# Kernel tuning notes

Measured on AMD Instinct MI355X. Metric: run time of the kernel, lower is better.

## Reference

```python
import jax, jax.numpy as jnp
import numpy as np

N, E, D, H = 100000, 640000, 128, 256


def _mlp(x, w1, b1, w2, b2, w3, b3):
    x = jax.nn.relu(x @ w1.T + b1)
    x = jax.nn.relu(x @ w2.T + b2)
    return x @ w3.T + b3


def _gru(x, h, wih, whh, bih, bhh):
    gi = x @ wih.T + bih
    gh = h @ whh.T + bhh
    ir, iz, inn = jnp.split(gi, 3, axis=-1)
    hr, hz, hn = jnp.split(gh, 3, axis=-1)
    r = jax.nn.sigmoid(ir + hr)
    z = jax.nn.sigmoid(iz + hz)
    n = jnp.tanh(inn + r * hn)
    return (1.0 - z) * n + z * h


def setup_inputs() -> dict:
    key = jax.random.key(0)
    ks = jax.random.split(key, 24)
    s = lambda *shape: 0.05
    inp = {
        "node_states": jax.random.normal(ks[0], (N, D), jnp.float32),
        "edge_features": jax.random.normal(ks[1], (E, D), jnp.float32),
        "from_idx": jax.random.randint(ks[2], (E,), 0, N, jnp.int64 if jax.config.jax_enable_x64 else jnp.int32),
        "to_idx": jax.random.randint(ks[3], (E,), 0, N, jnp.int64 if jax.config.jax_enable_x64 else jnp.int32),
        "graph_idx": jax.random.randint(ks[4], (N,), 0, 16, jnp.int32),
        # message_net MLP params
        "w1": jax.random.normal(ks[5], (H, 3 * D), jnp.float32) * 0.05,
        "b1": jnp.zeros((H,), jnp.float32),
        "w2": jax.random.normal(ks[6], (H, H), jnp.float32) * 0.05,
        "b2": jnp.zeros((H,), jnp.float32),
        "w3": jax.random.normal(ks[7], (D, H), jnp.float32) * 0.05,
        "b3": jnp.zeros((D,), jnp.float32),
    }
    # three GRU cells
    for i in range(3):
        inp[f"g{i}_wih"] = jax.random.normal(ks[8 + 4 * i], (3 * D, D), jnp.float32) * 0.05
        inp[f"g{i}_whh"] = jax.random.normal(ks[9 + 4 * i], (3 * D, D), jnp.float32) * 0.05
        inp[f"g{i}_bih"] = jnp.zeros((3 * D,), jnp.float32)
        inp[f"g{i}_bhh"] = jnp.zeros((3 * D,), jnp.float32)
    return inp


def _prop_once(node_states, f_idx, t_idx, edge_features, w1, b1, w2, b2, w3, b3):
    from_states = node_states[f_idx]  # [E, D]
    to_states = node_states[t_idx]    # [E, D]
    edge_inputs = jnp.concatenate([from_states, to_states, edge_features], axis=1)  # [E, 3D]
    edge_states = _mlp(edge_inputs, w1, b1, w2, b2, w3, b3)  # [E, D]
    return jax.ops.segment_sum(edge_states, t_idx, num_segments=node_states.shape[0])


def reference(node_states, edge_features, from_idx, to_idx, graph_idx,
              w1, b1, w2, b2, w3, b3,
              g0_wih, g0_whh, g0_bih, g0_bhh,
              g1_wih, g1_whh, g1_bih, g1_bhh,
              g2_wih, g2_whh, g2_bih, g2_bhh):
    # both directions use self.message_net in the original forward
    agg = _prop_once(node_states, from_idx, to_idx, edge_features, w1, b1, w2, b2, w3, b3)
    agg = agg + _prop_once(node_states, to_idx, from_idx, edge_features, w1, b1, w2, b2, w3, b3)
    s1 = _gru(node_states, agg, g0_wih, g0_whh, g0_bih, g0_bhh)
    s2 = _gru(agg, s1, g1_wih, g1_whh, g1_bih, g1_bhh)
    s3 = _gru(s1, s2, g2_wih, g2_whh, g2_bih, g2_bhh)
    return s3
```

## Files before the change

### kernel.cpp

```cpp
#include <hip/hip_runtime.h>

#define NN 100000
#define NE 640000
#define D 128
#define HH 256
#define TD 384

typedef __bf16 bf16x8 __attribute__((ext_vector_type(8)));
typedef float f32x4 __attribute__((ext_vector_type(4)));

__device__ __forceinline__ unsigned short f2bf(float f) {
    unsigned u = __builtin_bit_cast(unsigned, f);
    u += 0x7FFFu + ((u >> 16) & 1u);
    return (unsigned short)(u >> 16);
}

__global__ void cvt_bf16_kernel(const float* __restrict__ src,
                                unsigned short* __restrict__ dst, int n) {
    int i = blockIdx.x * 256 + threadIdx.x;
    if (i < n) dst[i] = f2bf(src[i]);
}

__global__ __launch_bounds__(256, 2) void edge_mlp_kernel(
    const float* __restrict__ ns, const float* __restrict__ ef,
    const int* __restrict__ fidx, const int* __restrict__ tidx,
    const unsigned short* __restrict__ w1b, const float* __restrict__ b1,
    const unsigned short* __restrict__ w2b, const float* __restrict__ b2,
    const unsigned short* __restrict__ w3b, const float* __restrict__ b3,
    float* __restrict__ agg)
{
    __shared__ __align__(16) unsigned short chunks[96 * 128];
    __shared__ __align__(16) unsigned short hbuf[64 * 256];
    __shared__ int sF[32], sT[32];

    const int tid = threadIdx.x;
    const int e0 = blockIdx.x * 32;
    if (tid < 32) { sF[tid] = fidx[e0 + tid]; sT[tid] = tidx[e0 + tid]; }
    __syncthreads();

    {
        const int kk0 = (tid & 7) * 16;
        for (int c = tid >> 3; c < 96; c += 32) {
            const int edge = c & 31;
            const int part = c >> 5;
            const float* src = (part == 0) ? ns + (size_t)sF[edge] * D
                             : (part == 1) ? ns + (size_t)sT[edge] * D
                                           : ef + (size_t)(e0 + edge) * D;
            unsigned short* cb = chunks + c * 128;
            #pragma unroll
            for (int g = 0; g < 2; g++) {
                float4 a = *(const float4*)(src + kk0 + g * 8);
                float4 b = *(const float4*)(src + kk0 + g * 8 + 4);
                uint4 pk;
                pk.x = f2bf(a.x) | ((unsigned)f2bf(a.y) << 16);
                pk.y = f2bf(a.z) | ((unsigned)f2bf(a.w) << 16);
                pk.z = f2bf(b.x) | ((unsigned)f2bf(b.y) << 16);
                pk.w = f2bf(b.z) | ((unsigned)f2bf(b.w) << 16);
                int sw = (kk0 + g * 8) ^ ((edge & 7) << 3);
                *(uint4*)(cb + sw) = pk;
            }
        }
    }
    __syncthreads();

    const int w  = tid >> 6;
    const int l  = tid & 63;
    const int lr = l & 15;
    const int lk = l >> 4;

    f32x4 acc1[4][4];
    #pragma unroll
    for (int mt = 0; mt < 4; mt++)
        #pragma unroll
        for (int ct = 0; ct < 4; ct++) acc1[mt][ct] = (f32x4){0.f, 0.f, 0.f, 0.f};

    for (int kc = 0; kc < 12; kc++) {
        const int gk = kc * 32;
        const int c128 = gk >> 7;
        const int kk = (gk & 127) + lk * 8;
        bf16x8 af[4];
        #pragma unroll
        for (int mt = 0; mt < 4; mt++) {
            int edge = ((mt & 1) << 4) + lr;
            int dir = mt >> 1;
            int part = dir ? (c128 == 0 ? 1 : (c128 == 1 ? 0 : 2)) : c128;
            int idx = (part * 32 + edge) * 128 + (kk ^ ((edge & 7) << 3));
            af[mt] = *(const bf16x8*)(chunks + idx);
        }
        #pragma unroll
        for (int ct = 0; ct < 4; ct++) {
            int col = (w * 4 + ct) * 16 + lr;
            bf16x8 bfr = *(const bf16x8*)(w1b + col * TD + gk + lk * 8);
            #pragma unroll
            for (int mt = 0; mt < 4; mt++)
                acc1[mt][ct] = __builtin_amdgcn_mfma_f32_16x16x32_bf16(af[mt], bfr, acc1[mt][ct], 0, 0, 0);
        }
    }
    #pragma unroll
    for (int ct = 0; ct < 4; ct++) {
        int col = (w * 4 + ct) * 16 + lr;
        float bias = b1[col];
        #pragma unroll
        for (int mt = 0; mt < 4; mt++)
            #pragma unroll
            for (int j = 0; j < 4; j++) {
                int row = mt * 16 + lk * 4 + j;
                float v = acc1[mt][ct][j] + bias;
                v = v > 0.f ? v : 0.f;
                hbuf[row * 256 + (col ^ ((row & 7) << 3))] = f2bf(v);
            }
    }
    __syncthreads();

    f32x4 acc2[4][4];
    #pragma unroll
    for (int mt = 0; mt < 4; mt++)
        #pragma unroll
        for (int ct = 0; ct < 4; ct++) acc2[mt][ct] = (f32x4){0.f, 0.f, 0.f, 0.f};

    for (int kc = 0; kc < 8; kc++) {
        const int k = kc * 32 + lk * 8;
        bf16x8 af[4];
        #pragma unroll
        for (int mt = 0; mt < 4; mt++) {
            int row = mt * 16 + lr;
            af[mt] = *(const bf16x8*)(hbuf + row * 256 + (k ^ ((row & 7) << 3)));
        }
        #pragma unroll
        for (int ct = 0; ct < 4; ct++) {
            int col = (w * 4 + ct) * 16 + lr;
            bf16x8 bfr = *(const bf16x8*)(w2b + col * 256 + k);
            #pragma unroll
            for (int mt = 0; mt < 4; mt++)
                acc2[mt][ct] = __builtin_amdgcn_mfma_f32_16x16x32_bf16(af[mt], bfr, acc2[mt][ct], 0, 0, 0);
        }
    }
    __syncthreads();
    #pragma unroll
    for (int ct = 0; ct < 4; ct++) {
        int col = (w * 4 + ct) * 16 + lr;
        float bias = b2[col];
        #pragma unroll
        for (int mt = 0; mt < 4; mt++)
            #pragma unroll
            for (int j = 0; j < 4; j++) {
                int row = mt * 16 + lk * 4 + j;
                float v = acc2[mt][ct][j] + bias;
                v = v > 0.f ? v : 0.f;
                hbuf[row * 256 + (col ^ ((row & 7) << 3))] = f2bf(v);
            }
    }
    __syncthreads();

    f32x4 acc3[4][2];
    #pragma unroll
    for (int mt = 0; mt < 4; mt++) { acc3[mt][0] = (f32x4){0.f,0.f,0.f,0.f}; acc3[mt][1] = (f32x4){0.f,0.f,0.f,0.f}; }

    for (int kc = 0; kc < 8; kc++) {
        const int k = kc * 32 + lk * 8;
        bf16x8 af[4];
        #pragma unroll
        for (int mt = 0; mt < 4; mt++) {
            int row = mt * 16 + lr;
            af[mt] = *(const bf16x8*)(hbuf + row * 256 + (k ^ ((row & 7) << 3)));
        }
        #pragma unroll
        for (int ct = 0; ct < 2; ct++) {
            int col = (w * 2 + ct) * 16 + lr;
            bf16x8 bfr = *(const bf16x8*)(w3b + col * 256 + k);
            #pragma unroll
            for (int mt = 0; mt < 4; mt++)
                acc3[mt][ct] = __builtin_amdgcn_mfma_f32_16x16x32_bf16(af[mt], bfr, acc3[mt][ct], 0, 0, 0);
        }
    }

    #pragma unroll
    for (int ct = 0; ct < 2; ct++) {
        int d = (w * 2 + ct) * 16 + lr;
        float bias = b3[d];
        #pragma unroll
        for (int mt = 0; mt < 4; mt++)
            #pragma unroll
            for (int j = 0; j < 4; j++) {
                int edge = ((mt & 1) << 4) + lk * 4 + j;
                int node = (mt >> 1) ? sF[edge] : sT[edge];
                atomicAdd(agg + (size_t)node * D + d, acc3[mt][ct][j] + bias);
            }
    }
}

__global__ __launch_bounds__(256, 2) void gru_kernel(
    const float* __restrict__ x, const float* __restrict__ h,
    const unsigned short* __restrict__ wihb, const unsigned short* __restrict__ whhb,
    const float* __restrict__ bih, const float* __restrict__ bhh,
    float* __restrict__ out)
{
    __shared__ __align__(16) unsigned short xb[32 * 128];
    __shared__ __align__(16) unsigned short hb[32 * 128];
    const int tid = threadIdx.x;
    const size_t r0 = (size_t)blockIdx.x * 32;

    {
        const int row = tid >> 3;
        const int kk0 = (tid & 7) * 16;
        const float* sx = x + (r0 + row) * D + kk0;
        const float* sh = h + (r0 + row) * D + kk0;
        #pragma unroll
        for (int g = 0; g < 2; g++) {
            float4 a = *(const float4*)(sx + g * 8);
            float4 b = *(const float4*)(sx + g * 8 + 4);
            uint4 pk;
            pk.x = f2bf(a.x) | ((unsigned)f2bf(a.y) << 16);
            pk.y = f2bf(a.z) | ((unsigned)f2bf(a.w) << 16);
            pk.z = f2bf(b.x) | ((unsigned)f2bf(b.y) << 16);
            pk.w = f2bf(b.z) | ((unsigned)f2bf(b.w) << 16);
            int sw = (kk0 + g * 8) ^ ((row & 7) << 3);
            *(uint4*)(xb + row * 128 + sw) = pk;
            a = *(const float4*)(sh + g * 8);
            b = *(const float4*)(sh + g * 8 + 4);
            pk.x = f2bf(a.x) | ((unsigned)f2bf(a.y) << 16);
            pk.y = f2bf(a.z) | ((unsigned)f2bf(a.w) << 16);
            pk.z = f2bf(b.x) | ((unsigned)f2bf(b.y) << 16);
            pk.w = f2bf(b.z) | ((unsigned)f2bf(b.w) << 16);
            *(uint4*)(hb + row * 128 + sw) = pk;
        }
    }
    __syncthreads();

    const int w = tid >> 6, l = tid & 63, lr = l & 15, lk = l >> 4;

    f32x4 agi[2][3][2], agh[2][3][2];
    #pragma unroll
    for (int mt = 0; mt < 2; mt++)
        #pragma unroll
        for (int g = 0; g < 3; g++)
            #pragma unroll
            for (int t = 0; t < 2; t++) {
                agi[mt][g][t] = (f32x4){0.f,0.f,0.f,0.f};
                agh[mt][g][t] = (f32x4){0.f,0.f,0.f,0.f};
            }

    for (int kc = 0; kc < 4; kc++) {
        const int k = kc * 32 + lk * 8;
        bf16x8 ax[2], ah[2];
        #pragma unroll
        for (int mt = 0; mt < 2; mt++) {
            int row = mt * 16 + lr;
            int idx = row * 128 + (k ^ ((row & 7) << 3));
            ax[mt] = *(const bf16x8*)(xb + idx);
            ah[mt] = *(const bf16x8*)(hb + idx);
        }
        #pragma unroll
        for (int g = 0; g < 3; g++)
            #pragma unroll
            for (int t = 0; t < 2; t++) {
                int col = g * 128 + (w * 2 + t) * 16 + lr;
                bf16x8 bi = *(const bf16x8*)(wihb + col * 128 + k);
                bf16x8 bh = *(const bf16x8*)(whhb + col * 128 + k);
                #pragma unroll
                for (int mt = 0; mt < 2; mt++) {
                    agi[mt][g][t] = __builtin_amdgcn_mfma_f32_16x16x32_bf16(ax[mt], bi, agi[mt][g][t], 0, 0, 0);
                    agh[mt][g][t] = __builtin_amdgcn_mfma_f32_16x16x32_bf16(ah[mt], bh, agh[mt][g][t], 0, 0, 0);
                }
            }
    }

    #pragma unroll
    for (int t = 0; t < 2; t++) {
        const int d = (w * 2 + t) * 16 + lr;
        const float bir = bih[d], biz = bih[D + d], bin_ = bih[2 * D + d];
        const float bhr = bhh[d], bhz = bhh[D + d], bhn = bhh[2 * D + d];
        #pragma unroll
        for (int mt = 0; mt < 2; mt++)
            #pragma unroll
            for (int j = 0; j < 4; j++) {
                size_t row = r0 + mt * 16 + lk * 4 + j;
                float hv = h[row * D + d];
                float rr = agi[mt][0][t][j] + bir + agh[mt][0][t][j] + bhr;
                float zz = agi[mt][1][t][j] + biz + agh[mt][1][t][j] + bhz;
                float ni = agi[mt][2][t][j] + bin_;
                float nh = agh[mt][2][t][j] + bhn;
                float r_ = 1.f / (1.f + __expf(-rr));
                float z_ = 1.f / (1.f + __expf(-zz));
                float n_ = tanhf(ni + r_ * nh);
                out[row * D + d] = (1.f - z_) * n_ + z_ * hv;
            }
    }
}

extern "C" void kernel_launch(void* const* d_in, const int* in_sizes, int n_in,
                              void* d_out, int out_size, void* d_ws, size_t ws_size,
                              hipStream_t stream)
{
    const float* ns = (const float*)d_in[0];
    const float* ef = (const float*)d_in[1];
    const int*   fidx = (const int*)d_in[2];
    const int*   tidx = (const int*)d_in[3];
    const float* w1 = (const float*)d_in[5];
    const float* b1 = (const float*)d_in[6];
    const float* w2 = (const float*)d_in[7];
    const float* b2 = (const float*)d_in[8];
    const float* w3 = (const float*)d_in[9];
    const float* b3 = (const float*)d_in[10];
    const float* gwih_f[3] = {(const float*)d_in[11], (const float*)d_in[15], (const float*)d_in[19]};
    const float* gwhh_f[3] = {(const float*)d_in[12], (const float*)d_in[16], (const float*)d_in[20]};
    const float* gbih[3]   = {(const float*)d_in[13], (const float*)d_in[17], (const float*)d_in[21]};
    const float* gbhh[3]   = {(const float*)d_in[14], (const float*)d_in[18], (const float*)d_in[22]};

    char* ws = (char*)d_ws;
    float* agg = (float*)ws;
    float* s1  = (float*)(ws + (size_t)NN * D * 4);
    unsigned short* w1b = (unsigned short*)(ws + (size_t)2 * NN * D * 4);
    unsigned short* w2b = w1b + 256 * 384;
    unsigned short* w3b = w2b + 256 * 256;
    unsigned short* gwih[3];
    unsigned short* gwhh[3];
    {
        unsigned short* p = w3b + 128 * 256;
        for (int i = 0; i < 3; i++) { gwih[i] = p; p += 384 * 128; gwhh[i] = p; p += 384 * 128; }
    }

    auto cvt = [&](const float* s, unsigned short* dst, int n) {
        cvt_bf16_kernel<<<(n + 255) / 256, 256, 0, stream>>>(s, dst, n);
    };
    cvt(w1, w1b, 256 * 384);
    cvt(w2, w2b, 256 * 256);
    cvt(w3, w3b, 128 * 256);
    for (int i = 0; i < 3; i++) { cvt(gwih_f[i], gwih[i], 384 * 128); cvt(gwhh_f[i], gwhh[i], 384 * 128); }

    hipMemsetAsync(agg, 0, (size_t)NN * D * 4, stream);

    edge_mlp_kernel<<<NE / 32, 256, 0, stream>>>(ns, ef, fidx, tidx, w1b, b1, w2b, b2, w3b, b3, agg);

    float* s2 = (float*)d_out;
    gru_kernel<<<NN / 32, 256, 0, stream>>>(ns,  agg, gwih[0], gwhh[0], gbih[0], gbhh[0], s1);
    gru_kernel<<<NN / 32, 256, 0, stream>>>(agg, s1,  gwih[1], gwhh[1], gbih[1], gbhh[1], s2);
    gru_kernel<<<NN / 32, 256, 0, stream>>>(s1,  s2,  gwih[2], gwhh[2], gbih[2], gbhh[2], (float*)d_out);
}
```

Baseline: 1.690 ms.

## Pre-convert node/edge features to bf16 and gather via direct global-to-LDS loads

Converts node states and edge features to bf16 once up front, then gathers them into shared memory with global_load_lds 16-byte transfers instead of loading fp32 and converting per block. It also merges the chunk and hidden shared buffers into one array (adding a barrier) and raises the launch-bounds occupancy hint from 2 to 4. The aim is to halve gather bandwidth and raise occupancy, at the cost of an extra conversion pass over about 190 MB of fp32 input and a dependence on workspace size.

```diff
diff --git a/kernel.cpp b/kernel.cpp
--- a/kernel.cpp
+++ b/kernel.cpp
@@ -15,22 +15,36 @@
     return (unsigned short)(u >> 16);
 }
 
-__global__ void cvt_bf16_kernel(const float* __restrict__ src,
-                                unsigned short* __restrict__ dst, int n) {
+__device__ __forceinline__ void gl_lds16(const unsigned short* g, unsigned short* l) {
+    __builtin_amdgcn_global_load_lds((const __attribute__((address_space(1))) unsigned int*)g,
+                                     (__attribute__((address_space(3))) unsigned int*)l, 16, 0, 0);
+}
+
+__global__ void cvt8_kernel(const float* __restrict__ src,
+                            unsigned short* __restrict__ dst, int n8) {
     int i = blockIdx.x * 256 + threadIdx.x;
-    if (i < n) dst[i] = f2bf(src[i]);
-}
-
-__global__ __launch_bounds__(256, 2) void edge_mlp_kernel(
+    if (i >= n8) return;
+    const float4* s = (const float4*)(src + (size_t)i * 8);
+    float4 a = s[0], b = s[1];
+    uint4 pk;
+    pk.x = f2bf(a.x) | ((unsigned)f2bf(a.y) << 16);
+    pk.y = f2bf(a.z) | ((unsigned)f2bf(a.w) << 16);
+    pk.z = f2bf(b.x) | ((unsigned)f2bf(b.y) << 16);
+    pk.w = f2bf(b.z) | ((unsigned)f2bf(b.w) << 16);
+    *(uint4*)(dst + (size_t)i * 8) = pk;
+}
+
+template<bool PRE>
+__global__ __launch_bounds__(256, 4) void edge_mlp_v2(
     const float* __restrict__ ns, const float* __restrict__ ef,
+    const unsigned short* __restrict__ nsb, const unsigned short* __restrict__ efb,
     const int* __restrict__ fidx, const int* __restrict__ tidx,
     const unsigned short* __restrict__ w1b, const float* __restrict__ b1,
     const unsigned short* __restrict__ w2b, const float* __restrict__ b2,
     const unsigned short* __restrict__ w3b, const float* __restrict__ b3,
     float* __restrict__ agg)
 {
-    __shared__ __align__(16) unsigned short chunks[96 * 128];
-    __shared__ __align__(16) unsigned short hbuf[64 * 256];
+    __shared__ __align__(16) unsigned short smem[64 * 256];
     __shared__ int sF[32], sT[32];
 
     const int tid = threadIdx.x;
@@ -38,7 +52,25 @@
     if (tid < 32) { sF[tid] = fidx[e0 + tid]; sT[tid] = tidx[e0 + tid]; }
     __syncthreads();
 
-    {
+    const int w  = tid >> 6;
+    const int l  = tid & 63;
+    const int lr = l & 15;
+    const int lk = l >> 4;
+
+    if (PRE) {
+        #pragma unroll
+        for (int i = 0; i < 6; i++) {
+            int cbase = w * 24 + i * 4;
+            int c = cbase + (l >> 4);
+            int edge = c & 31, part = c >> 5;
+            int slot = (l & 15) ^ (edge & 7);
+            const unsigned short* src =
+                  (part == 0) ? nsb + (size_t)sF[edge] * 128
+                : (part == 1) ? nsb + (size_t)sT[edge] * 128
+                              : efb + (size_t)(e0 + edge) * 128;
+            gl_lds16(src + slot * 8, smem + cbase * 128);
+        }
+    } else {
         const int kk0 = (tid & 7) * 16;
         for (int c = tid >> 3; c < 96; c += 32) {
             const int edge = c & 31;
@@ -46,7 +78,7 @@
             const float* src = (part == 0) ? ns + (size_t)sF[edge] * D
                              : (part == 1) ? ns + (size_t)sT[edge] * D
                                            : ef + (size_t)(e0 + edge) * D;
-            unsigned short* cb = chunks + c * 128;
+            unsigned short* cb = smem + c * 128;
             #pragma unroll
             for (int g = 0; g < 2; g++) {
                 float4 a = *(const float4*)(src + kk0 + g * 8);
@@ -63,11 +95,6 @@
     }
     __syncthreads();
 
-    const int w  = tid >> 6;
-    const int l  = tid & 63;
-    const int lr = l & 15;
-    const int lk = l >> 4;
-
     f32x4 acc1[4][4];
     #pragma unroll
     for (int mt = 0; mt < 4; mt++)
@@ -85,7 +112,7 @@
             int dir = mt >> 1;
             int part = dir ? (c128 == 0 ? 1 : (c128 == 1 ? 0 : 2)) : c128;
             int idx = (part * 32 + edge) * 128 + (kk ^ ((edge & 7) << 3));
-            af[mt] = *(const bf16x8*)(chunks + idx);
+            af[mt] = *(const bf16x8*)(smem + idx);
         }
         #pragma unroll
         for (int ct = 0; ct < 4; ct++) {
@@ -96,6 +123,8 @@
                 acc1[mt][ct] = __builtin_amdgcn_mfma_f32_16x16x32_bf16(af[mt], bfr, acc1[mt][ct], 0, 0, 0);
         }
     }
+    __syncthreads();
+
     #pragma unroll
     for (int ct = 0; ct < 4; ct++) {
         int col = (w * 4 + ct) * 16 + lr;
@@ -107,7 +136,7 @@
                 int row = mt * 16 + lk * 4 + j;
                 float v = acc1[mt][ct][j] + bias;
                 v = v > 0.f ? v : 0.f;
-                hbuf[row * 256 + (col ^ ((row & 7) << 3))] = f2bf(v);
+                smem[row * 256 + (col ^ ((row & 7) << 3))] = f2bf(v);
             }
     }
     __syncthreads();
@@ -124,7 +153,7 @@
         #pragma unroll
         for (int mt = 0; mt < 4; mt++) {
             int row = mt * 16 + lr;
-            af[mt] = *(const bf16x8*)(hbuf + row * 256 + (k ^ ((row & 7) << 3)));
+            af[mt] = *(const bf16x8*)(smem + row * 256 + (k ^ ((row & 7) << 3)));
         }
         #pragma unroll
         for (int ct = 0; ct < 4; ct++) {
@@ -147,7 +176,7 @@
                 int row = mt * 16 + lk * 4 + j;
                 float v = acc2[mt][ct][j] + bias;
                 v = v > 0.f ? v : 0.f;
-                hbuf[row * 256 + (col ^ ((row & 7) << 3))] = f2bf(v);
+                smem[row * 256 + (col ^ ((row & 7) << 3))] = f2bf(v);
             }
     }
     __syncthreads();
@@ -162,7 +191,7 @@
         #pragma unroll
         for (int mt = 0; mt < 4; mt++) {
             int row = mt * 16 + lr;
-            af[mt] = *(const bf16x8*)(hbuf + row * 256 + (k ^ ((row & 7) << 3)));
+            af[mt] = *(const bf16x8*)(smem + row * 256 + (k ^ ((row & 7) << 3)));
         }
         #pragma unroll
         for (int ct = 0; ct < 2; ct++) {
@@ -315,22 +344,32 @@
     unsigned short* w3b = w2b + 256 * 256;
     unsigned short* gwih[3];
     unsigned short* gwhh[3];
-    {
-        unsigned short* p = w3b + 128 * 256;
-        for (int i = 0; i < 3; i++) { gwih[i] = p; p += 384 * 128; gwhh[i] = p; p += 384 * 128; }
-    }
-
-    auto cvt = [&](const float* s, unsigned short* dst, int n) {
-        cvt_bf16_kernel<<<(n + 255) / 256, 256, 0, stream>>>(s, dst, n);
+    unsigned short* p = w3b + 128 * 256;
+    for (int i = 0; i < 3; i++) { gwih[i] = p; p += 384 * 128; gwhh[i] = p; p += 384 * 128; }
+    unsigned short* nsb = p;
+    unsigned short* efb = nsb + (size_t)NN * D;
+    size_t needed = (size_t)((char*)(efb + (size_t)NE * D) - ws);
+    const bool pre = (ws_size >= needed);
+
+    auto cvt = [&](const float* s, unsigned short* dst, size_t n) {
+        int n8 = (int)(n / 8);
+        cvt8_kernel<<<(n8 + 255) / 256, 256, 0, stream>>>(s, dst, n8);
     };
     cvt(w1, w1b, 256 * 384);
     cvt(w2, w2b, 256 * 256);
     cvt(w3, w3b, 128 * 256);
     for (int i = 0; i < 3; i++) { cvt(gwih_f[i], gwih[i], 384 * 128); cvt(gwhh_f[i], gwhh[i], 384 * 128); }
+    if (pre) {
+        cvt(ns, nsb, (size_t)NN * D);
+        cvt(ef, efb, (size_t)NE * D);
+    }
 
     hipMemsetAsync(agg, 0, (size_t)NN * D * 4, stream);
 
-    edge_mlp_kernel<<<NE / 32, 256, 0, stream>>>(ns, ef, fidx, tidx, w1b, b1, w2b, b2, w3b, b3, agg);
+    if (pre)
+        edge_mlp_v2<true><<<NE / 32, 256, 0, stream>>>(ns, ef, nsb, efb, fidx, tidx, w1b, b1, w2b, b2, w3b, b3, agg);
+    else
+        edge_mlp_v2<false><<<NE / 32, 256, 0, stream>>>(ns, ef, nsb, efb, fidx, tidx, w1b, b1, w2b, b2, w3b, b3, agg);
 
     float* s2 = (float*)d_out;
     gru_kernel<<<NN / 32, 256, 0, stream>>>(ns,  agg, gwih[0], gwhh[0], gbih[0], gbhh[0], s1);
```

Result: slower. 2.016 ms (+19.3%).

## Warp-specialize edge MLP with ping-pong halves overlapping gather and compute

Applied to the files above, without the earlier changes.

The edge MLP kernel becomes persistent-ish: each 512-thread block processes 10 edge tiles, with the two 256-thread halves alternating roles. One half runs the three MFMA layers for the current tile while the other gathers and converts the next tile's node and edge features into a double-buffered LDS chunk. This is meant to hide the irregular gather latency behind matrix work, at the cost of more LDS, extra block-wide barriers, and half the threads idle for compute at any time. The weight conversion kernel is also vectorized to 8 elements per thread.

```diff
diff --git a/kernel.cpp b/kernel.cpp
--- a/kernel.cpp
+++ b/kernel.cpp
@@ -5,6 +5,7 @@
 #define D 128
 #define HH 256
 #define TD 384
+#define TPB 10
 
 typedef __bf16 bf16x8 __attribute__((ext_vector_type(8)));
 typedef float f32x4 __attribute__((ext_vector_type(4)));
@@ -15,13 +16,24 @@
     return (unsigned short)(u >> 16);
 }
 
-__global__ void cvt_bf16_kernel(const float* __restrict__ src,
-                                unsigned short* __restrict__ dst, int n) {
+__device__ __forceinline__ uint4 pack8(float4 a, float4 b) {
+    uint4 pk;
+    pk.x = f2bf(a.x) | ((unsigned)f2bf(a.y) << 16);
+    pk.y = f2bf(a.z) | ((unsigned)f2bf(a.w) << 16);
+    pk.z = f2bf(b.x) | ((unsigned)f2bf(b.y) << 16);
+    pk.w = f2bf(b.z) | ((unsigned)f2bf(b.w) << 16);
+    return pk;
+}
+
+__global__ void cvt8_kernel(const float* __restrict__ src,
+                            unsigned short* __restrict__ dst, int n8) {
     int i = blockIdx.x * 256 + threadIdx.x;
-    if (i < n) dst[i] = f2bf(src[i]);
-}
-
-__global__ __launch_bounds__(256, 2) void edge_mlp_kernel(
+    if (i >= n8) return;
+    const float4* s = (const float4*)(src + (size_t)i * 8);
+    *(uint4*)(dst + (size_t)i * 8) = pack8(s[0], s[1]);
+}
+
+__global__ __launch_bounds__(512, 2) void edge_mlp_v8(
     const float* __restrict__ ns, const float* __restrict__ ef,
     const int* __restrict__ fidx, const int* __restrict__ tidx,
     const unsigned short* __restrict__ w1b, const float* __restrict__ b1,
@@ -29,163 +41,220 @@
     const unsigned short* __restrict__ w3b, const float* __restrict__ b3,
     float* __restrict__ agg)
 {
-    __shared__ __align__(16) unsigned short chunks[96 * 128];
+    __shared__ __align__(16) unsigned short chunks[2][96 * 128];
     __shared__ __align__(16) unsigned short hbuf[64 * 256];
-    __shared__ int sF[32], sT[32];
-
-    const int tid = threadIdx.x;
-    const int e0 = blockIdx.x * 32;
-    if (tid < 32) { sF[tid] = fidx[e0 + tid]; sT[tid] = tidx[e0 + tid]; }
+    __shared__ int sIdx[4][2][32];
+
+    const int tid  = threadIdx.x;
+    const int half = tid >> 8;
+    const int t256 = tid & 255;
+    const int tile0 = blockIdx.x * TPB;
+
+    if (tid < 32) {
+        sIdx[0][0][tid] = fidx[tile0 * 32 + tid];
+        sIdx[0][1][tid] = tidx[tile0 * 32 + tid];
+    } else if (tid < 64) {
+        int e = tid - 32;
+        sIdx[1][0][e] = fidx[(tile0 + 1) * 32 + e];
+        sIdx[1][1][e] = tidx[(tile0 + 1) * 32 + e];
+    }
     __syncthreads();
 
+    #pragma unroll
+    for (int k = 0; k < 2; k++) {
+        int u = tid + k * 512;
+        int c = u >> 4, s = u & 15, edge = c & 31;
+        int node = (c < 32) ? sIdx[0][0][edge] : sIdx[0][1][edge];
+        const float* src = ns + (size_t)node * 128 + s * 8;
+        float4 a = *(const float4*)(src);
+        float4 b = *(const float4*)(src + 4);
+        *(uint4*)(chunks[0] + c * 128 + ((s * 8) ^ ((edge & 7) << 3))) = pack8(a, b);
+    }
     {
-        const int kk0 = (tid & 7) * 16;
-        for (int c = tid >> 3; c < 96; c += 32) {
-            const int edge = c & 31;
-            const int part = c >> 5;
-            const float* src = (part == 0) ? ns + (size_t)sF[edge] * D
-                             : (part == 1) ? ns + (size_t)sT[edge] * D
-                                           : ef + (size_t)(e0 + edge) * D;
-            unsigned short* cb = chunks + c * 128;
-            #pragma unroll
-            for (int g = 0; g < 2; g++) {
-                float4 a = *(const float4*)(src + kk0 + g * 8);
-                float4 b = *(const float4*)(src + kk0 + g * 8 + 4);
-                uint4 pk;
-                pk.x = f2bf(a.x) | ((unsigned)f2bf(a.y) << 16);
-                pk.y = f2bf(a.z) | ((unsigned)f2bf(a.w) << 16);
-                pk.z = f2bf(b.x) | ((unsigned)f2bf(b.y) << 16);
-                pk.w = f2bf(b.z) | ((unsigned)f2bf(b.w) << 16);
-                int sw = (kk0 + g * 8) ^ ((edge & 7) << 3);
-                *(uint4*)(cb + sw) = pk;
-            }
-        }
-    }
-    __syncthreads();
-
-    const int w  = tid >> 6;
-    const int l  = tid & 63;
+        int u = tid;
+        int row = u >> 4, s = u & 15;
+        const float* src = ef + ((size_t)tile0 * 32 + row) * 128 + s * 8;
+        float4 a = *(const float4*)(src);
+        float4 b = *(const float4*)(src + 4);
+        *(uint4*)(chunks[0] + (64 + row) * 128 + ((s * 8) ^ ((row & 7) << 3))) = pack8(a, b);
+    }
+
+    const int w  = t256 >> 6;
+    const int l  = t256 & 63;
     const int lr = l & 15;
     const int lk = l >> 4;
 
-    f32x4 acc1[4][4];
-    #pragma unroll
-    for (int mt = 0; mt < 4; mt++)
-        #pragma unroll
-        for (int ct = 0; ct < 4; ct++) acc1[mt][ct] = (f32x4){0.f, 0.f, 0.f, 0.f};
-
-    for (int kc = 0; kc < 12; kc++) {
-        const int gk = kc * 32;
-        const int c128 = gk >> 7;
-        const int kk = (gk & 127) + lk * 8;
-        bf16x8 af[4];
-        #pragma unroll
-        for (int mt = 0; mt < 4; mt++) {
-            int edge = ((mt & 1) << 4) + lr;
-            int dir = mt >> 1;
-            int part = dir ? (c128 == 0 ? 1 : (c128 == 1 ? 0 : 2)) : c128;
-            int idx = (part * 32 + edge) * 128 + (kk ^ ((edge & 7) << 3));
-            af[mt] = *(const bf16x8*)(chunks + idx);
-        }
-        #pragma unroll
-        for (int ct = 0; ct < 4; ct++) {
-            int col = (w * 4 + ct) * 16 + lr;
-            bf16x8 bfr = *(const bf16x8*)(w1b + col * TD + gk + lk * 8);
+    int cur = 0;
+    for (int i = 0; i < TPB; i++) {
+        const bool comp = ((i & 1) == half);
+        float4 nst[8], est[4];
+        f32x4 acc1[4][4], acc2[4][4], acc3[4][2];
+
+        __syncthreads();
+
+        if (comp) {
             #pragma unroll
             for (int mt = 0; mt < 4; mt++)
-                acc1[mt][ct] = __builtin_amdgcn_mfma_f32_16x16x32_bf16(af[mt], bfr, acc1[mt][ct], 0, 0, 0);
-        }
-    }
-    #pragma unroll
-    for (int ct = 0; ct < 4; ct++) {
-        int col = (w * 4 + ct) * 16 + lr;
-        float bias = b1[col];
-        #pragma unroll
-        for (int mt = 0; mt < 4; mt++)
-            #pragma unroll
-            for (int j = 0; j < 4; j++) {
-                int row = mt * 16 + lk * 4 + j;
-                float v = acc1[mt][ct][j] + bias;
-                v = v > 0.f ? v : 0.f;
-                hbuf[row * 256 + (col ^ ((row & 7) << 3))] = f2bf(v);
-            }
-    }
-    __syncthreads();
-
-    f32x4 acc2[4][4];
-    #pragma unroll
-    for (int mt = 0; mt < 4; mt++)
-        #pragma unroll
-        for (int ct = 0; ct < 4; ct++) acc2[mt][ct] = (f32x4){0.f, 0.f, 0.f, 0.f};
-
-    for (int kc = 0; kc < 8; kc++) {
-        const int k = kc * 32 + lk * 8;
-        bf16x8 af[4];
-        #pragma unroll
-        for (int mt = 0; mt < 4; mt++) {
-            int row = mt * 16 + lr;
-            af[mt] = *(const bf16x8*)(hbuf + row * 256 + (k ^ ((row & 7) << 3)));
-        }
-        #pragma unroll
-        for (int ct = 0; ct < 4; ct++) {
-            int col = (w * 4 + ct) * 16 + lr;
-            bf16x8 bfr = *(const bf16x8*)(w2b + col * 256 + k);
+                #pragma unroll
+                for (int ct = 0; ct < 4; ct++) acc1[mt][ct] = (f32x4){0.f, 0.f, 0.f, 0.f};
+            for (int kc = 0; kc < 12; kc++) {
+                const int gk = kc * 32;
+                const int c128 = gk >> 7;
+                const int kk = (gk & 127) + lk * 8;
+                bf16x8 af[4];
+                #pragma unroll
+                for (int mt = 0; mt < 4; mt++) {
+                    int edge = ((mt & 1) << 4) + lr;
+                    int dir = mt >> 1;
+                    int part = dir ? (c128 == 0 ? 1 : (c128 == 1 ? 0 : 2)) : c128;
+                    int idx = (part * 32 + edge) * 128 + (kk ^ ((edge & 7) << 3));
+                    af[mt] = *(const bf16x8*)(chunks[cur] + idx);
+                }
+                #pragma unroll
+                for (int ct = 0; ct < 4; ct++) {
+                    int col = (w * 4 + ct) * 16 + lr;
+                    bf16x8 bfr = *(const bf16x8*)(w1b + col * TD + gk + lk * 8);
+                    #pragma unroll
+                    for (int mt = 0; mt < 4; mt++)
+                        acc1[mt][ct] = __builtin_amdgcn_mfma_f32_16x16x32_bf16(af[mt], bfr, acc1[mt][ct], 0, 0, 0);
+                }
+            }
+            #pragma unroll
+            for (int ct = 0; ct < 4; ct++) {
+                int col = (w * 4 + ct) * 16 + lr;
+                float bias = b1[col];
+                #pragma unroll
+                for (int mt = 0; mt < 4; mt++)
+                    #pragma unroll
+                    for (int j = 0; j < 4; j++) {
+                        int row = mt * 16 + lk * 4 + j;
+                        float v = acc1[mt][ct][j] + bias;
+                        v = v > 0.f ? v : 0.f;
+                        hbuf[row * 256 + (col ^ ((row & 7) << 3))] = f2bf(v);
+                    }
+            }
+        } else if (i + 1 < TPB) {
+            const int p1 = (i + 1) & 3;
+            #pragma unroll
+            for (int k = 0; k < 4; k++) {
+                int u = t256 + k * 256;
+                int c = u >> 4, s = u & 15, edge = c & 31;
+                int node = (c < 32) ? sIdx[p1][0][edge] : sIdx[p1][1][edge];
+                const float* src = ns + (size_t)node * 128 + s * 8;
+                nst[2 * k]     = *(const float4*)(src);
+                nst[2 * k + 1] = *(const float4*)(src + 4);
+            }
+            #pragma unroll
+            for (int k = 0; k < 2; k++) {
+                int u = t256 + k * 256;
+                int row = u >> 4, s = u & 15;
+                const float* src = ef + ((size_t)(tile0 + i + 1) * 32 + row) * 128 + s * 8;
+                est[2 * k]     = *(const float4*)(src);
+                est[2 * k + 1] = *(const float4*)(src + 4);
+            }
+            if (t256 < 32 && i + 2 < TPB) {
+                sIdx[(i + 2) & 3][0][t256] = fidx[(tile0 + i + 2) * 32 + t256];
+                sIdx[(i + 2) & 3][1][t256] = tidx[(tile0 + i + 2) * 32 + t256];
+            }
+        }
+        __syncthreads();
+
+        if (comp) {
             #pragma unroll
             for (int mt = 0; mt < 4; mt++)
-                acc2[mt][ct] = __builtin_amdgcn_mfma_f32_16x16x32_bf16(af[mt], bfr, acc2[mt][ct], 0, 0, 0);
-        }
-    }
-    __syncthreads();
-    #pragma unroll
-    for (int ct = 0; ct < 4; ct++) {
-        int col = (w * 4 + ct) * 16 + lr;
-        float bias = b2[col];
-        #pragma unroll
-        for (int mt = 0; mt < 4; mt++)
-            #pragma unroll
-            for (int j = 0; j < 4; j++) {
-                int row = mt * 16 + lk * 4 + j;
-                float v = acc2[mt][ct][j] + bias;
-                v = v > 0.f ? v : 0.f;
-                hbuf[row * 256 + (col ^ ((row & 7) << 3))] = f2bf(v);
-            }
-    }
-    __syncthreads();
-
-    f32x4 acc3[4][2];
-    #pragma unroll
-    for (int mt = 0; mt < 4; mt++) { acc3[mt][0] = (f32x4){0.f,0.f,0.f,0.f}; acc3[mt][1] = (f32x4){0.f,0.f,0.f,0.f}; }
-
-    for (int kc = 0; kc < 8; kc++) {
-        const int k = kc * 32 + lk * 8;
-        bf16x8 af[4];
-        #pragma unroll
-        for (int mt = 0; mt < 4; mt++) {
-            int row = mt * 16 + lr;
-            af[mt] = *(const bf16x8*)(hbuf + row * 256 + (k ^ ((row & 7) << 3)));
-        }
-        #pragma unroll
-        for (int ct = 0; ct < 2; ct++) {
-            int col = (w * 2 + ct) * 16 + lr;
-            bf16x8 bfr = *(const bf16x8*)(w3b + col * 256 + k);
-            #pragma unroll
-            for (int mt = 0; mt < 4; mt++)
-                acc3[mt][ct] = __builtin_amdgcn_mfma_f32_16x16x32_bf16(af[mt], bfr, acc3[mt][ct], 0, 0, 0);
-        }
-    }
-
-    #pragma unroll
-    for (int ct = 0; ct < 2; ct++) {
-        int d = (w * 2 + ct) * 16 + lr;
-        float bias = b3[d];
-        #pragma unroll
-        for (int mt = 0; mt < 4; mt++)
-            #pragma unroll
-            for (int j = 0; j < 4; j++) {
-                int edge = ((mt & 1) << 4) + lk * 4 + j;
-                int node = (mt >> 1) ? sF[edge] : sT[edge];
-                atomicAdd(agg + (size_t)node * D + d, acc3[mt][ct][j] + bias);
-            }
+                #pragma unroll
+                for (int ct = 0; ct < 4; ct++) acc2[mt][ct] = (f32x4){0.f, 0.f, 0.f, 0.f};
+            for (int kc = 0; kc < 8; kc++) {
+                const int k = kc * 32 + lk * 8;
+                bf16x8 af[4];
+                #pragma unroll
+                for (int mt = 0; mt < 4; mt++) {
+                    int row = mt * 16 + lr;
+                    af[mt] = *(const bf16x8*)(hbuf + row * 256 + (k ^ ((row & 7) << 3)));
+                }
+                #pragma unroll
+                for (int ct = 0; ct < 4; ct++) {
+                    int col = (w * 4 + ct) * 16 + lr;
+                    bf16x8 bfr = *(const bf16x8*)(w2b + col * 256 + k);
+                    #pragma unroll
+                    for (int mt = 0; mt < 4; mt++)
+                        acc2[mt][ct] = __builtin_amdgcn_mfma_f32_16x16x32_bf16(af[mt], bfr, acc2[mt][ct], 0, 0, 0);
+                }
+            }
+        } else if (i + 1 < TPB) {
+            #pragma unroll
+            for (int k = 0; k < 4; k++) {
+                int u = t256 + k * 256;
+                int c = u >> 4, s = u & 15, edge = c & 31;
+                *(uint4*)(chunks[cur ^ 1] + c * 128 + ((s * 8) ^ ((edge & 7) << 3))) = pack8(nst[2 * k], nst[2 * k + 1]);
+            }
+        }
+        __syncthreads();
+
+        if (comp) {
+            #pragma unroll
+            for (int ct = 0; ct < 4; ct++) {
+                int col = (w * 4 + ct) * 16 + lr;
+                float bias = b2[col];
+                #pragma unroll
+                for (int mt = 0; mt < 4; mt++)
+                    #pragma unroll
+                    for (int j = 0; j < 4; j++) {
+                        int row = mt * 16 + lk * 4 + j;
+                        float v = acc2[mt][ct][j] + bias;
+                        v = v > 0.f ? v : 0.f;
+                        hbuf[row * 256 + (col ^ ((row & 7) << 3))] = f2bf(v);
+                    }
+            }
+        } else if (i + 1 < TPB) {
+            #pragma unroll
+            for (int k = 0; k < 2; k++) {
+                int u = t256 + k * 256;
+                int row = u >> 4, s = u & 15;
+                *(uint4*)(chunks[cur ^ 1] + (64 + row) * 128 + ((s * 8) ^ ((row & 7) << 3))) = pack8(est[2 * k], est[2 * k + 1]);
+            }
+        }
+        __syncthreads();
+
+        if (comp) {
+            #pragma unroll
+            for (int mt = 0; mt < 4; mt++) {
+                acc3[mt][0] = (f32x4){0.f, 0.f, 0.f, 0.f};
+                acc3[mt][1] = (f32x4){0.f, 0.f, 0.f, 0.f};
+            }
+            for (int kc = 0; kc < 8; kc++) {
+                const int k = kc * 32 + lk * 8;
+                bf16x8 af[4];
+                #pragma unroll
+                for (int mt = 0; mt < 4; mt++) {
+                    int row = mt * 16 + lr;
+                    af[mt] = *(const bf16x8*)(hbuf + row * 256 + (k ^ ((row & 7) << 3)));
+                }
+                #pragma unroll
+                for (int ct = 0; ct < 2; ct++) {
+                    int col = (w * 2 + ct) * 16 + lr;
+                    bf16x8 bfr = *(const bf16x8*)(w3b + col * 256 + k);
+                    #pragma unroll
+                    for (int mt = 0; mt < 4; mt++)
+                        acc3[mt][ct] = __builtin_amdgcn_mfma_f32_16x16x32_bf16(af[mt], bfr, acc3[mt][ct], 0, 0, 0);
+                }
+            }
+            const int p = i & 3;
+            #pragma unroll
+            for (int ct = 0; ct < 2; ct++) {
+                int d = (w * 2 + ct) * 16 + lr;
+                float bias = b3[d];
+                #pragma unroll
+                for (int mt = 0; mt < 4; mt++)
+                    #pragma unroll
+                    for (int j = 0; j < 4; j++) {
+                        int edge = ((mt & 1) << 4) + lk * 4 + j;
+                        int node = (mt >> 1) ? sIdx[p][0][edge] : sIdx[p][1][edge];
+                        atomicAdd(agg + (size_t)node * D + d, acc3[mt][ct][j] + bias);
+                    }
+            }
+        }
+        cur ^= 1;
     }
 }
 
@@ -209,20 +278,11 @@
         for (int g = 0; g < 2; g++) {
             float4 a = *(const float4*)(sx + g * 8);
             float4 b = *(const float4*)(sx + g * 8 + 4);
-            uint4 pk;
-            pk.x = f2bf(a.x) | ((unsigned)f2bf(a.y) << 16);
-            pk.y = f2bf(a.z) | ((unsigned)f2bf(a.w) << 16);
-            pk.z = f2bf(b.x) | ((unsigned)f2bf(b.y) << 16);
-            pk.w = f2bf(b.z) | ((unsigned)f2bf(b.w) << 16);
             int sw = (kk0 + g * 8) ^ ((row & 7) << 3);
-            *(uint4*)(xb + row * 128 + sw) = pk;
+            *(uint4*)(xb + row * 128 + sw) = pack8(a, b);
             a = *(const float4*)(sh + g * 8);
             b = *(const float4*)(sh + g * 8 + 4);
-            pk.x = f2bf(a.x) | ((unsigned)f2bf(a.y) << 16);
-            pk.y = f2bf(a.z) | ((unsigned)f2bf(a.w) << 16);
-            pk.z = f2bf(b.x) | ((unsigned)f2bf(b.y) << 16);
-            pk.w = f2bf(b.z) | ((unsigned)f2bf(b.w) << 16);
-            *(uint4*)(hb + row * 128 + sw) = pk;
+            *(uint4*)(hb + row * 128 + sw) = pack8(a, b);
         }
     }
     __syncthreads();
@@ -315,13 +375,12 @@
     unsigned short* w3b = w2b + 256 * 256;
     unsigned short* gwih[3];
     unsigned short* gwhh[3];
-    {
-        unsigned short* p = w3b + 128 * 256;
-        for (int i = 0; i < 3; i++) { gwih[i] = p; p += 384 * 128; gwhh[i] = p; p += 384 * 128; }
-    }
-
-    auto cvt = [&](const float* s, unsigned short* dst, int n) {
-        cvt_bf16_kernel<<<(n + 255) / 256, 256, 0, stream>>>(s, dst, n);
+    unsigned short* p = w3b + 128 * 256;
+    for (int i = 0; i < 3; i++) { gwih[i] = p; p += 384 * 128; gwhh[i] = p; p += 384 * 128; }
+
+    auto cvt = [&](const float* s, unsigned short* dst, size_t n) {
+        int n8 = (int)(n / 8);
+        cvt8_kernel<<<(n8 + 255) / 256, 256, 0, stream>>>(s, dst, n8);
     };
     cvt(w1, w1b, 256 * 384);
     cvt(w2, w2b, 256 * 256);
@@ -330,7 +389,7 @@
 
     hipMemsetAsync(agg, 0, (size_t)NN * D * 4, stream);
 
-    edge_mlp_kernel<<<NE / 32, 256, 0, stream>>>(ns, ef, fidx, tidx, w1b, b1, w2b, b2, w3b, b3, agg);
+    edge_mlp_v8<<<NE / 32 / TPB, 512, 0, stream>>>(ns, ef, fidx, tidx, w1b, b1, w2b, b2, w3b, b3, agg);
 
     float* s2 = (float*)d_out;
     gru_kernel<<<NN / 32, 256, 0, stream>>>(ns,  agg, gwih[0], gwhh[0], gbih[0], gbhh[0], s1);
```

Measured after the change: 3.543 ms. 2.1x slower.

## Make edge MLP kernel persistent over tiles with register prefetch of next gather

Applied to the files above, without the earlier changes.

Each block now processes four 32-edge tiles in sequence. While layer 1 of the current tile computes, it issues global gathers for the next tile into registers, then writes them into the freed chunk buffer after the layer-1 barrier. This hides gather latency behind MFMA work and amortises block launch, at the cost of more registers, a quarter as many blocks, and extra barriers. Weight conversion also moves to a vectorised 8-element kernel.

```diff
diff --git a/kernel.cpp b/kernel.cpp
--- a/kernel.cpp
+++ b/kernel.cpp
@@ -5,6 +5,7 @@
 #define D 128
 #define HH 256
 #define TD 384
+#define TPB 4
 
 typedef __bf16 bf16x8 __attribute__((ext_vector_type(8)));
 typedef float f32x4 __attribute__((ext_vector_type(4)));
@@ -15,13 +16,24 @@
     return (unsigned short)(u >> 16);
 }
 
-__global__ void cvt_bf16_kernel(const float* __restrict__ src,
-                                unsigned short* __restrict__ dst, int n) {
+__device__ __forceinline__ uint4 pack8(float4 a, float4 b) {
+    uint4 pk;
+    pk.x = f2bf(a.x) | ((unsigned)f2bf(a.y) << 16);
+    pk.y = f2bf(a.z) | ((unsigned)f2bf(a.w) << 16);
+    pk.z = f2bf(b.x) | ((unsigned)f2bf(b.y) << 16);
+    pk.w = f2bf(b.z) | ((unsigned)f2bf(b.w) << 16);
+    return pk;
+}
+
+__global__ void cvt8_kernel(const float* __restrict__ src,
+                            unsigned short* __restrict__ dst, int n8) {
     int i = blockIdx.x * 256 + threadIdx.x;
-    if (i < n) dst[i] = f2bf(src[i]);
-}
-
-__global__ __launch_bounds__(256, 2) void edge_mlp_kernel(
+    if (i >= n8) return;
+    const float4* s = (const float4*)(src + (size_t)i * 8);
+    *(uint4*)(dst + (size_t)i * 8) = pack8(s[0], s[1]);
+}
+
+__global__ __launch_bounds__(256, 2) void edge_mlp_v9(
     const float* __restrict__ ns, const float* __restrict__ ef,
     const int* __restrict__ fidx, const int* __restrict__ tidx,
     const unsigned short* __restrict__ w1b, const float* __restrict__ b1,
@@ -31,161 +43,192 @@
 {
     __shared__ __align__(16) unsigned short chunks[96 * 128];
     __shared__ __align__(16) unsigned short hbuf[64 * 256];
-    __shared__ int sF[32], sT[32];
+    __shared__ int sIdx[4][2][32];
 
     const int tid = threadIdx.x;
-    const int e0 = blockIdx.x * 32;
-    if (tid < 32) { sF[tid] = fidx[e0 + tid]; sT[tid] = tidx[e0 + tid]; }
-    __syncthreads();
-
-    {
-        const int kk0 = (tid & 7) * 16;
-        for (int c = tid >> 3; c < 96; c += 32) {
-            const int edge = c & 31;
-            const int part = c >> 5;
-            const float* src = (part == 0) ? ns + (size_t)sF[edge] * D
-                             : (part == 1) ? ns + (size_t)sT[edge] * D
-                                           : ef + (size_t)(e0 + edge) * D;
-            unsigned short* cb = chunks + c * 128;
-            #pragma unroll
-            for (int g = 0; g < 2; g++) {
-                float4 a = *(const float4*)(src + kk0 + g * 8);
-                float4 b = *(const float4*)(src + kk0 + g * 8 + 4);
-                uint4 pk;
-                pk.x = f2bf(a.x) | ((unsigned)f2bf(a.y) << 16);
-                pk.y = f2bf(a.z) | ((unsigned)f2bf(a.w) << 16);
-                pk.z = f2bf(b.x) | ((unsigned)f2bf(b.y) << 16);
-                pk.w = f2bf(b.z) | ((unsigned)f2bf(b.w) << 16);
-                int sw = (kk0 + g * 8) ^ ((edge & 7) << 3);
-                *(uint4*)(cb + sw) = pk;
-            }
-        }
-    }
-    __syncthreads();
-
+    const int tile0 = blockIdx.x * TPB;
     const int w  = tid >> 6;
     const int l  = tid & 63;
     const int lr = l & 15;
     const int lk = l >> 4;
 
-    f32x4 acc1[4][4];
-    #pragma unroll
-    for (int mt = 0; mt < 4; mt++)
-        #pragma unroll
-        for (int ct = 0; ct < 4; ct++) acc1[mt][ct] = (f32x4){0.f, 0.f, 0.f, 0.f};
-
-    for (int kc = 0; kc < 12; kc++) {
-        const int gk = kc * 32;
-        const int c128 = gk >> 7;
-        const int kk = (gk & 127) + lk * 8;
-        bf16x8 af[4];
-        #pragma unroll
-        for (int mt = 0; mt < 4; mt++) {
-            int edge = ((mt & 1) << 4) + lr;
-            int dir = mt >> 1;
-            int part = dir ? (c128 == 0 ? 1 : (c128 == 1 ? 0 : 2)) : c128;
-            int idx = (part * 32 + edge) * 128 + (kk ^ ((edge & 7) << 3));
-            af[mt] = *(const bf16x8*)(chunks + idx);
+    {
+        const int e0 = tile0 * 32;
+        if (tid < 32) { sIdx[0][0][tid] = fidx[e0 + tid]; sIdx[0][1][tid] = tidx[e0 + tid]; }
+        #pragma unroll
+        for (int k = 0; k < 6; k++) {
+            int u = tid + k * 256, c = u >> 4, s = u & 15;
+            const float* src;
+            if (c < 64) {
+                int edge = c & 31;
+                int node = (c < 32) ? fidx[e0 + edge] : tidx[e0 + edge];
+                src = ns + (size_t)node * 128 + s * 8;
+            } else {
+                src = ef + ((size_t)e0 + (c - 64)) * 128 + s * 8;
+            }
+            float4 a = *(const float4*)src;
+            float4 b = *(const float4*)(src + 4);
+            *(uint4*)(chunks + c * 128 + ((s * 8) ^ ((c & 7) << 3))) = pack8(a, b);
+        }
+    }
+    __syncthreads();
+
+    for (int i = 0; i < TPB; i++) {
+        const bool more = (i + 1 < TPB);
+        float4 pf[6][2];
+        int nf = 0, nt = 0;
+
+        if (more) {
+            const int eb = (tile0 + i + 1) * 32;
+            if (tid < 32) { nf = fidx[eb + tid]; nt = tidx[eb + tid]; }
+            #pragma unroll
+            for (int k = 0; k < 6; k++) {
+                int u = tid + k * 256, c = u >> 4, s = u & 15;
+                const float* src;
+                if (c < 64) {
+                    int edge = c & 31;
+                    int node = (c < 32) ? fidx[eb + edge] : tidx[eb + edge];
+                    src = ns + (size_t)node * 128 + s * 8;
+                } else {
+                    src = ef + ((size_t)eb + (c - 64)) * 128 + s * 8;
+                }
+                pf[k][0] = *(const float4*)src;
+                pf[k][1] = *(const float4*)(src + 4);
+            }
+        }
+
+        f32x4 acc1[4][4];
+        #pragma unroll
+        for (int mt = 0; mt < 4; mt++)
+            #pragma unroll
+            for (int ct = 0; ct < 4; ct++) acc1[mt][ct] = (f32x4){0.f, 0.f, 0.f, 0.f};
+
+        for (int kc = 0; kc < 12; kc++) {
+            const int gk = kc * 32;
+            const int c128 = gk >> 7;
+            const int kk = (gk & 127) + lk * 8;
+            bf16x8 af[4];
+            #pragma unroll
+            for (int mt = 0; mt < 4; mt++) {
+                int edge = ((mt & 1) << 4) + lr;
+                int dir = mt >> 1;
+                int part = dir ? (c128 == 0 ? 1 : (c128 == 1 ? 0 : 2)) : c128;
+                int idx = (part * 32 + edge) * 128 + (kk ^ ((edge & 7) << 3));
+                af[mt] = *(const bf16x8*)(chunks + idx);
+            }
+            #pragma unroll
+            for (int ct = 0; ct < 4; ct++) {
+                int col = (w * 4 + ct) * 16 + lr;
+                bf16x8 bfr = *(const bf16x8*)(w1b + col * TD + gk + lk * 8);
+                #pragma unroll
+                for (int mt = 0; mt < 4; mt++)
+                    acc1[mt][ct] = __builtin_amdgcn_mfma_f32_16x16x32_bf16(af[mt], bfr, acc1[mt][ct], 0, 0, 0);
+            }
         }
         #pragma unroll
         for (int ct = 0; ct < 4; ct++) {
             int col = (w * 4 + ct) * 16 + lr;
-            bf16x8 bfr = *(const bf16x8*)(w1b + col * TD + gk + lk * 8);
+            float bias = b1[col];
             #pragma unroll
             for (int mt = 0; mt < 4; mt++)
-                acc1[mt][ct] = __builtin_amdgcn_mfma_f32_16x16x32_bf16(af[mt], bfr, acc1[mt][ct], 0, 0, 0);
-        }
-    }
-    #pragma unroll
-    for (int ct = 0; ct < 4; ct++) {
-        int col = (w * 4 + ct) * 16 + lr;
-        float bias = b1[col];
+                #pragma unroll
+                for (int j = 0; j < 4; j++) {
+                    int row = mt * 16 + lk * 4 + j;
+                    float v = acc1[mt][ct][j] + bias;
+                    v = v > 0.f ? v : 0.f;
+                    hbuf[row * 256 + (col ^ ((row & 7) << 3))] = f2bf(v);
+                }
+        }
+        __syncthreads();
+
+        if (more) {
+            #pragma unroll
+            for (int k = 0; k < 6; k++) {
+                int u = tid + k * 256, c = u >> 4, s = u & 15;
+                *(uint4*)(chunks + c * 128 + ((s * 8) ^ ((c & 7) << 3))) = pack8(pf[k][0], pf[k][1]);
+            }
+            if (tid < 32) { sIdx[(i + 1) & 3][0][tid] = nf; sIdx[(i + 1) & 3][1][tid] = nt; }
+        }
+
+        f32x4 acc2[4][4];
         #pragma unroll
         for (int mt = 0; mt < 4; mt++)
             #pragma unroll
-            for (int j = 0; j < 4; j++) {
-                int row = mt * 16 + lk * 4 + j;
-                float v = acc1[mt][ct][j] + bias;
-                v = v > 0.f ? v : 0.f;
-                hbuf[row * 256 + (col ^ ((row & 7) << 3))] = f2bf(v);
-            }
-    }
-    __syncthreads();
-
-    f32x4 acc2[4][4];
-    #pragma unroll
-    for (int mt = 0; mt < 4; mt++)
-        #pragma unroll
-        for (int ct = 0; ct < 4; ct++) acc2[mt][ct] = (f32x4){0.f, 0.f, 0.f, 0.f};
-
-    for (int kc = 0; kc < 8; kc++) {
-        const int k = kc * 32 + lk * 8;
-        bf16x8 af[4];
-        #pragma unroll
-        for (int mt = 0; mt < 4; mt++) {
-            int row = mt * 16 + lr;
-            af[mt] = *(const bf16x8*)(hbuf + row * 256 + (k ^ ((row & 7) << 3)));
-        }
+            for (int ct = 0; ct < 4; ct++) acc2[mt][ct] = (f32x4){0.f, 0.f, 0.f, 0.f};
+
+        for (int kc = 0; kc < 8; kc++) {
+            const int k = kc * 32 + lk * 8;
+            bf16x8 af[4];
+            #pragma unroll
+            for (int mt = 0; mt < 4; mt++) {
+                int row = mt * 16 + lr;
+                af[mt] = *(const bf16x8*)(hbuf + row * 256 + (k ^ ((row & 7) << 3)));
+            }
+            #pragma unroll
+            for (int ct = 0; ct < 4; ct++) {
+                int col = (w * 4 + ct) * 16 + lr;
+                bf16x8 bfr = *(const bf16x8*)(w2b + col * 256 + k);
+                #pragma unroll
+                for (int mt = 0; mt < 4; mt++)
+                    acc2[mt][ct] = __builtin_amdgcn_mfma_f32_16x16x32_bf16(af[mt], bfr, acc2[mt][ct], 0, 0, 0);
+            }
+        }
+        __syncthreads();
+
         #pragma unroll
         for (int ct = 0; ct < 4; ct++) {
             int col = (w * 4 + ct) * 16 + lr;
-            bf16x8 bfr = *(const bf16x8*)(w2b + col * 256 + k);
+            float bias = b2[col];
             #pragma unroll
             for (int mt = 0; mt < 4; mt++)
-                acc2[mt][ct] = __builtin_amdgcn_mfma_f32_16x16x32_bf16(af[mt], bfr, acc2[mt][ct], 0, 0, 0);
-        }
-    }
-    __syncthreads();
-    #pragma unroll
-    for (int ct = 0; ct < 4; ct++) {
-        int col = (w * 4 + ct) * 16 + lr;
-        float bias = b2[col];
-        #pragma unroll
-        for (int mt = 0; mt < 4; mt++)
-            #pragma unroll
-            for (int j = 0; j < 4; j++) {
-                int row = mt * 16 + lk * 4 + j;
-                float v = acc2[mt][ct][j] + bias;
-                v = v > 0.f ? v : 0.f;
-                hbuf[row * 256 + (col ^ ((row & 7) << 3))] = f2bf(v);
-            }
-    }
-    __syncthreads();
-
-    f32x4 acc3[4][2];
-    #pragma unroll
-    for (int mt = 0; mt < 4; mt++) { acc3[mt][0] = (f32x4){0.f,0.f,0.f,0.f}; acc3[mt][1] = (f32x4){0.f,0.f,0.f,0.f}; }
-
-    for (int kc = 0; kc < 8; kc++) {
-        const int k = kc * 32 + lk * 8;
-        bf16x8 af[4];
+                #pragma unroll
+                for (int j = 0; j < 4; j++) {
+                    int row = mt * 16 + lk * 4 + j;
+                    float v = acc2[mt][ct][j] + bias;
+                    v = v > 0.f ? v : 0.f;
+                    hbuf[row * 256 + (col ^ ((row & 7) << 3))] = f2bf(v);
+                }
+        }
+        __syncthreads();
+
+        f32x4 acc3[4][2];
         #pragma unroll
         for (int mt = 0; mt < 4; mt++) {
-            int row = mt * 16 + lr;
-            af[mt] = *(const bf16x8*)(hbuf + row * 256 + (k ^ ((row & 7) << 3)));
-        }
+            acc3[mt][0] = (f32x4){0.f, 0.f, 0.f, 0.f};
+            acc3[mt][1] = (f32x4){0.f, 0.f, 0.f, 0.f};
+        }
+        for (int kc = 0; kc < 8; kc++) {
+            const int k = kc * 32 + lk * 8;
+            bf16x8 af[4];
+            #pragma unroll
+            for (int mt = 0; mt < 4; mt++) {
+                int row = mt * 16 + lr;
+                af[mt] = *(const bf16x8*)(hbuf + row * 256 + (k ^ ((row & 7) << 3)));
+            }
+            #pragma unroll
+            for (int ct = 0; ct < 2; ct++) {
+                int col = (w * 2 + ct) * 16 + lr;
+                bf16x8 bfr = *(const bf16x8*)(w3b + col * 256 + k);
+                #pragma unroll
+                for (int mt = 0; mt < 4; mt++)
+                    acc3[mt][ct] = __builtin_amdgcn_mfma_f32_16x16x32_bf16(af[mt], bfr, acc3[mt][ct], 0, 0, 0);
+            }
+        }
+        __syncthreads();
+
         #pragma unroll
         for (int ct = 0; ct < 2; ct++) {
-            int col = (w * 2 + ct) * 16 + lr;
-            bf16x8 bfr = *(const bf16x8*)(w3b + col * 256 + k);
+            int d = (w * 2 + ct) * 16 + lr;
+            float bias = b3[d];
             #pragma unroll
             for (int mt = 0; mt < 4; mt++)
-                acc3[mt][ct] = __builtin_amdgcn_mfma_f32_16x16x32_bf16(af[mt], bfr, acc3[mt][ct], 0, 0, 0);
-        }
-    }
-
-    #pragma unroll
-    for (int ct = 0; ct < 2; ct++) {
-        int d = (w * 2 + ct) * 16 + lr;
-        float bias = b3[d];
-        #pragma unroll
-        for (int mt = 0; mt < 4; mt++)
-            #pragma unroll
-            for (int j = 0; j < 4; j++) {
-                int edge = ((mt & 1) << 4) + lk * 4 + j;
-                int node = (mt >> 1) ? sF[edge] : sT[edge];
-                atomicAdd(agg + (size_t)node * D + d, acc3[mt][ct][j] + bias);
-            }
+                #pragma unroll
+                for (int j = 0; j < 4; j++) {
+                    int edge = ((mt & 1) << 4) + lk * 4 + j;
+                    int node = (mt >> 1) ? sIdx[i & 3][0][edge] : sIdx[i & 3][1][edge];
+                    atomicAdd(agg + (size_t)node * D + d, acc3[mt][ct][j] + bias);
+                }
+        }
     }
 }
 
@@ -209,20 +252,11 @@
         for (int g = 0; g < 2; g++) {
             float4 a = *(const float4*)(sx + g * 8);
             float4 b = *(const float4*)(sx + g * 8 + 4);
-            uint4 pk;
-            pk.x = f2bf(a.x) | ((unsigned)f2bf(a.y) << 16);
-            pk.y = f2bf(a.z) | ((unsigned)f2bf(a.w) << 16);
-            pk.z = f2bf(b.x) | ((unsigned)f2bf(b.y) << 16);
-            pk.w = f2bf(b.z) | ((unsigned)f2bf(b.w) << 16);
             int sw = (kk0 + g * 8) ^ ((row & 7) << 3);
-            *(uint4*)(xb + row * 128 + sw) = pk;
+            *(uint4*)(xb + row * 128 + sw) = pack8(a, b);
             a = *(const float4*)(sh + g * 8);
             b = *(const float4*)(sh + g * 8 + 4);
-            pk.x = f2bf(a.x) | ((unsigned)f2bf(a.y) << 16);
-            pk.y = f2bf(a.z) | ((unsigned)f2bf(a.w) << 16);
-            pk.z = f2bf(b.x) | ((unsigned)f2bf(b.y) << 16);
-            pk.w = f2bf(b.z) | ((unsigned)f2bf(b.w) << 16);
-            *(uint4*)(hb + row * 128 + sw) = pk;
+            *(uint4*)(hb + row * 128 + sw) = pack8(a, b);
         }
     }
     __syncthreads();
@@ -315,13 +349,12 @@
     unsigned short* w3b = w2b + 256 * 256;
     unsigned short* gwih[3];
     unsigned short* gwhh[3];
-    {
-        unsigned short* p = w3b + 128 * 256;
-        for (int i = 0; i < 3; i++) { gwih[i] = p; p += 384 * 128; gwhh[i] = p; p += 384 * 128; }
-    }
-
-    auto cvt = [&](const float* s, unsigned short* dst, int n) {
-        cvt_bf16_kernel<<<(n + 255) / 256, 256, 0, stream>>>(s, dst, n);
+    unsigned short* p = w3b + 128 * 256;
+    for (int i = 0; i < 3; i++) { gwih[i] = p; p += 384 * 128; gwhh[i] = p; p += 384 * 128; }
+
+    auto cvt = [&](const float* s, unsigned short* dst, size_t n) {
+        int n8 = (int)(n / 8);
+        cvt8_kernel<<<(n8 + 255) / 256, 256, 0, stream>>>(s, dst, n8);
     };
     cvt(w1, w1b, 256 * 384);
     cvt(w2, w2b, 256 * 256);
@@ -330,7 +363,7 @@
 
     hipMemsetAsync(agg, 0, (size_t)NN * D * 4, stream);
 
-    edge_mlp_kernel<<<NE / 32, 256, 0, stream>>>(ns, ef, fidx, tidx, w1b, b1, w2b, b2, w3b, b3, agg);
+    edge_mlp_v9<<<NE / 32 / TPB, 256, 0, stream>>>(ns, ef, fidx, tidx, w1b, b1, w2b, b2, w3b, b3, agg);
 
     float* s2 = (float*)d_out;
     gru_kernel<<<NN / 32, 256, 0, stream>>>(ns,  agg, gwih[0], gwhh[0], gbih[0], gbhh[0], s1);
```

Result: slower. 3.993 ms (+136.2%).
